# Performance work log

Hardware: AMD Instinct MI355X
Metric: run time of the kernel (lower is better)

The kernel has to match this reference:

```python
import jax, jax.numpy as jnp
import numpy as np

N = 50000
E = 800000
IN_DIM = 128
HID = 128
OUT_DIM = 128
H = 16
D = OUT_DIM // H  # head_dim = 8
EF = 4
RF = 20
KV_IN = 2 * IN_DIM + EF + RF  # 280
EPS = 1e-5


def _layernorm(x, w, b):
    mu = jnp.mean(x, axis=-1, keepdims=True)
    var = jnp.var(x, axis=-1, keepdims=True)
    return (x - mu) * jax.lax.rsqrt(var + EPS) * w + b


def _mlp(x, W1, b1, ln_w, ln_b, W2, b2):
    # Linear -> LayerNorm -> ReLU -> Linear (num_layer=2, norm=True)
    hdn = x @ W1 + b1
    hdn = jax.nn.relu(_layernorm(hdn, ln_w, ln_b))
    return hdn @ W2 + b2


def _lin_init(key, fan_in, fan_out):
    k1, k2 = jax.random.split(key)
    s = 1.0 / np.sqrt(fan_in)
    W = jax.random.uniform(k1, (fan_in, fan_out), jnp.float32, -s, s)
    b = jax.random.uniform(k2, (fan_out,), jnp.float32, -s, s)
    return W, b


def _mlp_params(key, in_dim, hid, out_dim):
    k1, k2 = jax.random.split(key)
    W1, b1 = _lin_init(k1, in_dim, hid)
    W2, b2 = _lin_init(k2, hid, out_dim)
    return W1, b1, jnp.ones((hid,), jnp.float32), jnp.zeros((hid,), jnp.float32), W2, b2


def setup_inputs() -> dict:
    key = jax.random.key(0)
    ks = jax.random.split(key, 10)
    h = jax.random.normal(ks[0], (N, IN_DIM), jnp.float32)
    rel_x = jax.random.normal(ks[1], (E, 3), jnp.float32)
    r_feat = jax.random.normal(ks[2], (E, RF), jnp.float32)
    edge_feat = jax.random.normal(ks[3], (E, EF), jnp.float32)
    edge_index = jax.random.randint(ks[4], (2, E), 0, N, jnp.int64)

    xk = _mlp_params(ks[5], KV_IN, HID, OUT_DIM)
    xv = _mlp_params(ks[6], KV_IN, HID, H)
    xq = _mlp_params(ks[7], IN_DIM, HID, OUT_DIM)
    ew_W, ew_b = _lin_init(ks[8], RF, 1)

    d = {"h": h, "rel_x": rel_x, "r_feat": r_feat, "edge_feat": edge_feat,
         "edge_index": edge_index, "ew_W": ew_W, "ew_b": ew_b}
    for name, p in (("xk", xk), ("xv", xv), ("xq", xq)):
        d[name + "_W1"], d[name + "_b1"], d[name + "_ln_w"], d[name + "_ln_b"], d[name + "_W2"], d[name + "_b2"] = p
    return d


def reference(h, rel_x, r_feat, edge_feat, edge_index,
              ew_W, ew_b,
              xk_W1, xk_b1, xk_ln_w, xk_ln_b, xk_W2, xk_b2,
              xv_W1, xv_b1, xv_ln_w, xv_ln_b, xv_W2, xv_b2,
              xq_W1, xq_b1, xq_ln_w, xq_ln_b, xq_W2, xq_b2):
    src, dst = edge_index[0], edge_index[1]
    hi = h[dst]  # [E, IN_DIM]
    hj = h[src]  # [E, IN_DIM]
    kv_input = jnp.concatenate([edge_feat, r_feat, hi, hj], axis=-1)  # [E, KV_IN]

    k = _mlp(kv_input, xk_W1, xk_b1, xk_ln_w, xk_ln_b, xk_W2, xk_b2).reshape(E, H, D)
    v = _mlp(kv_input, xv_W1, xv_b1, xv_ln_w, xv_ln_b, xv_W2, xv_b2)  # [E, H]
    e_w = jax.nn.sigmoid(r_feat @ ew_W + ew_b)  # [E, 1]
    v = (v * e_w)[:, :, None] * rel_x[:, None, :]  # [E, H, 3]

    q = _mlp(h, xq_W1, xq_b1, xq_ln_w, xq_ln_b, xq_W2, xq_b2).reshape(N, H, D)
    scores = jnp.sum(q[dst] * k, axis=-1) / np.sqrt(D)  # [E, H]

    # scatter_softmax over destination groups
    seg_max = jax.ops.segment_max(scores, dst, num_segments=N)  # [N, H]
    ex = jnp.exp(scores - seg_max[dst])
    denom = jax.ops.segment_sum(ex, dst, num_segments=N)  # [N, H]
    alpha = ex / denom[dst]  # [E, H]

    m = alpha[:, :, None] * v  # [E, H, 3]
    output = jax.ops.segment_sum(m, dst, num_segments=N)  # [N, H, 3]
    return output.mean(axis=1)  # [N, 3]
```

## Files before the change

kernel.cpp:

```cpp
#include <hip/hip_runtime.h>
#include <hip/hip_bf16.h>

#define NN 50000
#define EE 800000
#define ET 32
#define SCB 49

typedef unsigned int u32;
typedef __attribute__((ext_vector_type(8))) short short8;
typedef __attribute__((ext_vector_type(4))) float floatx4;

template<bool BF>
__device__ __forceinline__ float ldf(const void* p, int i){
  if constexpr (BF) return __bfloat162float(((const __hip_bfloat16*)p)[i]);
  else              return ((const float*)p)[i];
}
__device__ __forceinline__ int gidx(const int* ei, int pos, bool i64){
  return i64 ? ei[2*pos] : ei[pos];
}
__device__ __forceinline__ bool det_bf(const void* lnw){
  return ((const u32*)lnw)[0] == 0x3F803F80u;
}
__device__ __forceinline__ bool det_i64(const int* ei){
  return ((ei[1] | ei[3] | ei[5] | ei[7]) == 0);
}

__device__ __forceinline__ unsigned short f2bf(float f){
  u32 u = __float_as_uint(f);
  u32 r = u + 0x7FFFu + ((u>>16)&1u);
  return (unsigned short)(r>>16);
}
__device__ __forceinline__ float bf2f(unsigned short s){
  return __uint_as_float(((u32)s)<<16);
}
__device__ __forceinline__ u32 cvtpk(float lo, float hi){
  u32 r;
  asm("v_cvt_pk_bf16_f32 %0, %1, %2" : "=v"(r) : "v"(lo), "v"(hi));
  return r;
}

__global__ void __launch_bounds__(256)
k_hist(const int* ei, int* cnt){
  int t = blockIdx.x*256 + threadIdx.x;
  if (t >= EE) return;
  bool i64 = det_i64(ei);
  atomicAdd(&cnt[gidx(ei, EE + t, i64)], 1);
}

__global__ void __launch_bounds__(256)
k_scan1(const int* cnt, int* bsum){
  __shared__ int wsum[4];
  int t=threadIdx.x, lane=t&63, wv=t>>6;
  int i0 = blockIdx.x*1024 + t*4;
  int s=0;
  #pragma unroll
  for(int j=0;j<4;j++){ int i=i0+j; s += (i<NN)?cnt[i]:0; }
  #pragma unroll
  for(int d=1;d<64;d<<=1) s += __shfl_xor(s,d);
  if(lane==0) wsum[wv]=s;
  __syncthreads();
  if(t==0) bsum[blockIdx.x]=wsum[0]+wsum[1]+wsum[2]+wsum[3];
}

__global__ void __launch_bounds__(256)
k_scan3(const int* cnt, const int* bsum, int* off){
  __shared__ int wsum[4];
  int t=threadIdx.x, lane=t&63, wv=t>>6;
  int base=0;
  for(int k=0;k<blockIdx.x;k++) base += bsum[k];
  int i0=blockIdx.x*1024 + t*4;
  int v0=(i0+0<NN)?cnt[i0+0]:0;
  int v1=(i0+1<NN)?cnt[i0+1]:0;
  int v2=(i0+2<NN)?cnt[i0+2]:0;
  int v3=(i0+3<NN)?cnt[i0+3]:0;
  int s=v0+v1+v2+v3;
  int sc=s;
  #pragma unroll
  for(int d=1;d<64;d<<=1){ int u=__shfl_up(sc,d); if(lane>=d) sc+=u; }
  if(lane==63) wsum[wv]=sc;
  __syncthreads();
  int wb=base;
  for(int k=0;k<wv;k++) wb+=wsum[k];
  int excl=wb+sc-s;
  if(i0+0<NN) off[i0+0]=excl;
  if(i0+1<NN) off[i0+1]=excl+v0;
  if(i0+2<NN) off[i0+2]=excl+v0+v1;
  if(i0+3<NN) off[i0+3]=excl+v0+v1+v2;
  if (blockIdx.x==SCB-1 && t==0)
    off[NN] = base + wsum[0]+wsum[1]+wsum[2]+wsum[3];
}

template<bool BF>
__device__ void scat_body(const int* ei, bool i64, const int* off, int* cur,
                          const void* rfeat, const void* relx,
                          const void* ewW, const void* ewb, float* blob){
  int t = blockIdx.x*256 + threadIdx.x;
  if (t >= EE) return;
  int d = gidx(ei, EE + t, i64);
  int pos = off[d] + atomicAdd(&cur[d], 1);
  float rf[20];
  if constexpr (!BF){
    const float* rp = (const float*)rfeat + (size_t)t*20;
    #pragma unroll
    for (int q=0;q<5;q++){
      float4 v4 = *(const float4*)(rp + q*4);
      rf[q*4+0]=v4.x; rf[q*4+1]=v4.y; rf[q*4+2]=v4.z; rf[q*4+3]=v4.w;
    }
  } else {
    #pragma unroll
    for (int j=0;j<20;j++) rf[j] = ldf<BF>(rfeat, t*20+j);
  }
  float aw = ldf<BF>(ewb, 0);
  #pragma unroll
  for (int j=0;j<20;j++) aw = fmaf(rf[j], ldf<BF>(ewW,j), aw);
  int4 a; a.x=d; a.y=gidx(ei, t, i64); a.z=t; a.w=0;
  float4 b;
  b.x = (1.f/(1.f + expf(-aw))) * (1.f/16.f);
  b.y = ldf<BF>(relx, t*3+0);
  b.z = ldf<BF>(relx, t*3+1);
  b.w = ldf<BF>(relx, t*3+2);
  ((int4*)blob)[2*(size_t)pos]   = a;
  ((float4*)blob)[2*(size_t)pos+1] = b;
}
__global__ void __launch_bounds__(256)
k_scat(const int* ei, const int* off, int* cur,
       const void* rfeat, const void* relx, const void* ewW, const void* ewb,
       float* blob, const void* lnw){
  bool i64 = det_i64(ei);
  if (det_bf(lnw)) scat_body<true >(ei,i64,off,cur,rfeat,relx,ewW,ewb,blob);
  else             scat_body<false>(ei,i64,off,cur,rfeat,relx,ewW,ewb,blob);
}

__global__ void __launch_bounds__(256)
k_wprep(const void* kW1, const void* vW1, const void* kW2, const void* vW2,
        const void* qW1, const void* qW2,
        unsigned short* w1sh, unsigned short* w1sl,
        unsigned short* w1nh, unsigned short* w1nl,
        unsigned short* w2kh, unsigned short* w2kl,
        unsigned short* w2vh, unsigned short* w2vl,
        unsigned short* w1qh, unsigned short* w1ql,
        unsigned short* w2qh, unsigned short* w2ql, const void* lnw){
  int idx = blockIdx.x*256 + threadIdx.x;
  bool bf = det_bf(lnw);
  {
    int c = idx>>7, k = idx&127;
    int row = (c<256) ? (24+k) : (152+k);
    int cc  = c & 127;
    const void* W = ((c&255)<128) ? kW1 : vW1;
    float f = bf ? __bfloat162float(((const __hip_bfloat16*)W)[row*128+cc]) : ((const float*)W)[row*128+cc];
    unsigned short h = f2bf(f); w1nh[idx]=h; w1nl[idx]=f2bf(f - bf2f(h));
  }
  if (idx < 16384){ int c = idx>>7, k = idx&127;
    { float f = bf ? __bfloat162float(((const __hip_bfloat16*)kW2)[k*128+c]) : ((const float*)kW2)[k*128+c];
      unsigned short h = f2bf(f); w2kh[idx]=h; w2kl[idx]=f2bf(f - bf2f(h)); }
    { float f = bf ? __bfloat162float(((const __hip_bfloat16*)qW1)[k*128+c]) : ((const float*)qW1)[k*128+c];
      unsigned short h = f2bf(f); w1qh[idx]=h; w1ql[idx]=f2bf(f - bf2f(h)); }
    { float f = bf ? __bfloat162float(((const __hip_bfloat16*)qW2)[k*128+c]) : ((const float*)qW2)[k*128+c];
      unsigned short h = f2bf(f); w2qh[idx]=h; w2ql[idx]=f2bf(f - bf2f(h)); }
  }
  if (idx < 2048){ int c = idx>>7, k = idx&127;
    float f = bf ? __bfloat162float(((const __hip_bfloat16*)vW2)[k*16+c]) : ((const float*)vW2)[k*16+c];
    unsigned short h = f2bf(f); w2vh[idx]=h; w2vl[idx]=f2bf(f - bf2f(h)); }
  if (idx < 8192){ int c = idx>>5, k = idx&31;
    float f = 0.f;
    if (k < 24){
      if (c < 128) f = bf ? __bfloat162float(((const __hip_bfloat16*)kW1)[k*128+c]) : ((const float*)kW1)[k*128+c];
      else         f = bf ? __bfloat162float(((const __hip_bfloat16*)vW1)[k*128+(c-128)]) : ((const float*)vW1)[k*128+(c-128)];
    }
    unsigned short h = f2bf(f); w1sh[idx]=h; w1sl[idx]=f2bf(f - bf2f(h)); }
}

template<bool BF>
__device__ void nodeq_body(const void* h,
                           const unsigned short* w1nh, const unsigned short* w1nl,
                           const unsigned short* w1qh, const unsigned short* w1ql,
                           const unsigned short* w2qh, const unsigned short* w2ql,
                           const void* kb1, const void* vb1,
                           const void* qb1, const void* qlnw, const void* qlnb, const void* qb2,
                           float* hkd, float* hks, float* qws,
                           unsigned short* xh, unsigned short* xl,
                           unsigned short* yh, unsigned short* yl,
                           float2 (*lnred)[4]){
  const int t = threadIdx.x;
  const int n0 = blockIdx.x*16;
  const int lane = t&63, w = t>>6;
  const int arow = lane&15, agrp = lane>>4;
  { int nd = t>>4, c8 = (t&15)*8;
    float v[8];
    if constexpr (!BF){
      float4 a = *(const float4*)&((const float*)h)[(n0+nd)*128 + c8];
      float4 b = *(const float4*)&((const float*)h)[(n0+nd)*128 + c8 + 4];
      v[0]=a.x; v[1]=a.y; v[2]=a.z; v[3]=a.w; v[4]=b.x; v[5]=b.y; v[6]=b.z; v[7]=b.w;
    } else {
      short8 raw = *(const short8*)&((const __hip_bfloat16*)h)[(n0+nd)*128 + c8];
      #pragma unroll
      for (int i=0;i<8;i++) v[i] = bf2f((unsigned short)raw[i]);
    }
    short8 hv, lv;
    #pragma unroll
    for (int i=0;i<8;i++){
      unsigned short hh = f2bf(v[i]);
      hv[i] = (short)hh; lv[i] = (short)f2bf(v[i]-bf2f(hh));
    }
    int sidx = (nd*128 + c8) ^ ((nd&7)<<3);
    *(short8*)&xh[sidx] = hv;
    *(short8*)&xl[sidx] = lv;
  }
  __syncthreads();
  { floatx4 acc[8];
    #pragma unroll
    for (int ct=0; ct<8; ct++)
      #pragma unroll
      for (int r=0;r<4;r++) acc[ct][r]=0.f;
    #pragma unroll
    for (int ks=0; ks<4; ks++){
      int aidx = (arow*128 + ks*32 + agrp*8) ^ ((arow&7)<<3);
      short8 Ah = *(const short8*)&xh[aidx];
      short8 Al = *(const short8*)&xl[aidx];
      #pragma unroll
      for (int ct=0; ct<8; ct++){
        int gc = w*128 + ct*16 + arow;
        short8 Bh = *(const short8*)&w1nh[gc*128 + ks*32 + agrp*8];
        short8 Bl = *(const short8*)&w1nl[gc*128 + ks*32 + agrp*8];
        acc[ct] = __builtin_amdgcn_mfma_f32_16x16x32_bf16(Ah, Bh, acc[ct], 0,0,0);
        acc[ct] = __builtin_amdgcn_mfma_f32_16x16x32_bf16(Al, Bh, acc[ct], 0,0,0);
        acc[ct] = __builtin_amdgcn_mfma_f32_16x16x32_bf16(Ah, Bl, acc[ct], 0,0,0);
      }
    }
    if (w < 2){
      #pragma unroll
      for (int ct=0; ct<8; ct++){
        int gc = w*128 + ct*16 + arow;
        float bb = (gc<128) ? ldf<BF>(kb1,gc) : ldf<BF>(vb1,gc-128);
        #pragma unroll
        for (int r=0;r<4;r++) acc[ct][r] += bb;
      }
    }
    float* base = (w<2) ? hkd : hks;
    const int ob = (w&1)*128;
    #pragma unroll
    for (int r=0;r<4;r++){
      int n = n0 + agrp*4 + r;
      float4 lo4 = make_float4(acc[0][r],acc[1][r],acc[2][r],acc[3][r]);
      float4 hi4 = make_float4(acc[4][r],acc[5][r],acc[6][r],acc[7][r]);
      *(float4*)&base[(size_t)n*256 + ob + arow*4]      = lo4;
      *(float4*)&base[(size_t)n*256 + ob + 64 + arow*4] = hi4;
    }
  }
  floatx4 Cq[2];
  #pragma unroll
  for (int nt=0; nt<2; nt++){
    int col = w*32 + nt*16 + arow;
    float bb = ldf<BF>(qb1, col);
    #pragma unroll
    for (int r=0;r<4;r++) Cq[nt][r] = bb;
  }
  #pragma unroll
  for (int ks=0; ks<4; ks++){
    int aidx = (arow*128 + ks*32 + agrp*8) ^ ((arow&7)<<3);
    short8 Ah = *(const short8*)&xh[aidx];
    short8 Al = *(const short8*)&xl[aidx];
    #pragma unroll
    for (int nt=0; nt<2; nt++){
      int col = w*32 + nt*16 + arow;
      short8 Bh = *(const short8*)&w1qh[col*128 + ks*32 + agrp*8];
      short8 Bl = *(const short8*)&w1ql[col*128 + ks*32 + agrp*8];
      Cq[nt] = __builtin_amdgcn_mfma_f32_16x16x32_bf16(Ah, Bh, Cq[nt], 0,0,0);
      Cq[nt] = __builtin_amdgcn_mfma_f32_16x16x32_bf16(Al, Bh, Cq[nt], 0,0,0);
      Cq[nt] = __builtin_amdgcn_mfma_f32_16x16x32_bf16(Ah, Bl, Cq[nt], 0,0,0);
    }
  }
  { float s1[4], s2[4];
    #pragma unroll
    for (int r=0;r<4;r++){ s1[r]=0.f; s2[r]=0.f; }
    #pragma unroll
    for (int nt=0; nt<2; nt++)
      #pragma unroll
      for (int r=0;r<4;r++){ float v=Cq[nt][r]; s1[r]+=v; s2[r]=fmaf(v,v,s2[r]); }
    #pragma unroll
    for (int d=1; d<16; d<<=1){
      #pragma unroll
      for (int r=0;r<4;r++){ s1[r]+=__shfl_xor(s1[r],d); s2[r]+=__shfl_xor(s2[r],d); }
    }
    if (arow==0){
      #pragma unroll
      for (int r=0;r<4;r++) lnred[agrp*4+r][w] = make_float2(s1[r], s2[r]);
    }
  }
  __syncthreads();
  float mu[4], rs[4];
  #pragma unroll
  for (int r=0;r<4;r++){
    int row = agrp*4+r;
    float s=0.f, q=0.f;
    #pragma unroll
    for (int k=0;k<4;k++){ float2 p=lnred[row][k]; s+=p.x; q+=p.y; }
    float m = s*(1.f/128.f);
    mu[r]=m; rs[r]=rsqrtf(q*(1.f/128.f) - m*m + 1e-5f);
  }
  #pragma unroll
  for (int nt=0; nt<2; nt++){
    int col = w*32 + nt*16 + arow;
    float lw = ldf<BF>(qlnw, col), lb = ldf<BF>(qlnb, col);
    #pragma unroll
    for (int r=0;r<4;r++){
      int row = agrp*4+r;
      float v = fmaxf((Cq[nt][r]-mu[r])*rs[r]*lw + lb, 0.f);
      unsigned short hh = f2bf(v);
      int idx = (row*128 + col) ^ ((row&7)<<3);
      yh[idx] = hh;
      yl[idx] = f2bf(v - bf2f(hh));
    }
  }
  __syncthreads();
  floatx4 Co[2];
  #pragma unroll
  for (int nt=0; nt<2; nt++){
    int col = w*32 + nt*16 + arow;
    float bb = ldf<BF>(qb2, col);
    #pragma unroll
    for (int r=0;r<4;r++) Co[nt][r] = bb;
  }
  #pragma unroll
  for (int ks=0; ks<4; ks++){
    int aidx = (arow*128 + ks*32 + agrp*8) ^ ((arow&7)<<3);
    short8 Ah = *(const short8*)&yh[aidx];
    short8 Al = *(const short8*)&yl[aidx];
    #pragma unroll
    for (int nt=0; nt<2; nt++){
      int col = w*32 + nt*16 + arow;
      short8 Bh = *(const short8*)&w2qh[col*128 + ks*32 + agrp*8];
      short8 Bl = *(const short8*)&w2ql[col*128 + ks*32 + agrp*8];
      Co[nt] = __builtin_amdgcn_mfma_f32_16x16x32_bf16(Ah, Bh, Co[nt], 0,0,0);
      Co[nt] = __builtin_amdgcn_mfma_f32_16x16x32_bf16(Al, Bh, Co[nt], 0,0,0);
      Co[nt] = __builtin_amdgcn_mfma_f32_16x16x32_bf16(Ah, Bl, Co[nt], 0,0,0);
    }
  }
  #pragma unroll
  for (int r=0;r<4;r++){
    int n = n0 + agrp*4 + r;
    *(float2*)&qws[(size_t)n*128 + w*32 + arow*2] = make_float2(Co[0][r], Co[1][r]);
  }
}
__global__ void __launch_bounds__(256)
k_nodeq(const void* h,
        const unsigned short* w1nh, const unsigned short* w1nl,
        const unsigned short* w1qh, const unsigned short* w1ql,
        const unsigned short* w2qh, const unsigned short* w2ql,
        const void* kb1, const void* vb1,
        const void* qb1, const void* qlnw, const void* qlnb, const void* qb2,
        float* hkd, float* hks, float* qws){
  __shared__ unsigned short xh[16*128];
  __shared__ unsigned short xl[16*128];
  __shared__ unsigned short yh[16*128];
  __shared__ unsigned short yl[16*128];
  __shared__ float2 lnred[16][4];
  if (det_bf(qlnw)) nodeq_body<true >(h,w1nh,w1nl,w1qh,w1ql,w2qh,w2ql,kb1,vb1,qb1,qlnw,qlnb,qb2,hkd,hks,qws,xh,xl,yh,yl,lnred);
  else              nodeq_body<false>(h,w1nh,w1nl,w1qh,w1ql,w2qh,w2ql,kb1,vb1,qb1,qlnw,qlnb,qb2,hkd,hks,qws,xh,xl,yh,yl,lnred);
}

template<bool BF>
__device__ void edge_body(const void* rfeat, const void* efeat, const float* blob,
                          const void* klnw, const void* klnb,
                          const void* vlnw, const void* vlnb,
                          const void* kb2, const void* vb2,
                          const unsigned short* w1sh, const unsigned short* w1sl,
                          const unsigned short* w2kh, const unsigned short* w2kl,
                          const unsigned short* w2vh, const unsigned short* w2vl,
                          const float* hkd, const float* hks, const float* qws,
                          float* scw, float* vsw,
                          unsigned short* ahi, unsigned short* sfh,
                          int* dste, int* srce, float* ewv,
                          float2 (*lnred)[4], float* sc_lds){
  const int t  = threadIdx.x;
  const int e0 = blockIdx.x*ET;
  const int lane = t&63, w = t>>6;
  const int arow = lane&15, agrp = lane>>4;
  const int* bi = (const int*)blob;

  if (t < ET)             dste[t]     = bi[(size_t)(e0+t)*8 + 0];
  else if (t < 2*ET)      srce[t-ET]  = bi[(size_t)(e0+t-ET)*8 + 1];
  else if (t < 3*ET)      ewv[t-2*ET] = blob[(size_t)(e0+t-2*ET)*8 + 4];
  #pragma unroll
  for (int it=0; it<4; it++){
    int id = it*256+t; int e = id>>5, j = id&31;
    int ge = bi[(size_t)(e0+e)*8 + 2];
    float f = (j<4) ? ldf<BF>(efeat, ge*4+j)
            : (j<24 ? ldf<BF>(rfeat, ge*20+(j-4)) : 0.f);
    sfh[e*40+j] = f2bf(f);
  }
  __syncthreads();

  const int wcol = w*64 + arow;
  const int pbase = w*64 + arow*4;
  floatx4 C[2][4];
  #pragma unroll
  for (int g=0; g<2; g++){
    #pragma unroll
    for (int r=0;r<4;r++){
      int e = g*16 + agrp*4 + r;
      float4 gd = *(const float4*)&hkd[(size_t)(u32)dste[e]*256u + pbase];
      float4 gs = *(const float4*)&hks[(size_t)(u32)srce[e]*256u + pbase];
      C[g][0][r] = gd.x+gs.x; C[g][1][r] = gd.y+gs.y;
      C[g][2][r] = gd.z+gs.z; C[g][3][r] = gd.w+gs.w;
    }
  }
  #pragma unroll
  for (int g=0; g<2; g++){
    short8 Ah = *(const short8*)&sfh[(g*16+arow)*40 + agrp*8];
    #pragma unroll
    for (int nt=0; nt<4; nt++){
      const int col = wcol + nt*16;
      short8 Bh = *(const short8*)&w1sh[col*32 + agrp*8];
      short8 Bl = *(const short8*)&w1sl[col*32 + agrp*8];
      C[g][nt] = __builtin_amdgcn_mfma_f32_16x16x32_bf16(Ah, Bh, C[g][nt], 0,0,0);
      C[g][nt] = __builtin_amdgcn_mfma_f32_16x16x32_bf16(Ah, Bl, C[g][nt], 0,0,0);
    }
  }
  #pragma unroll
  for (int g=0; g<2; g++){
    float s1[4], s2[4];
    #pragma unroll
    for (int r=0;r<4;r++){ s1[r]=0.f; s2[r]=0.f; }
    #pragma unroll
    for (int nt=0; nt<4; nt++)
      #pragma unroll
      for (int r=0;r<4;r++){ float v=C[g][nt][r]; s1[r]+=v; s2[r]=fmaf(v,v,s2[r]); }
    #pragma unroll
    for (int d=1; d<16; d<<=1){
      #pragma unroll
      for (int r=0;r<4;r++){ s1[r]+=__shfl_xor(s1[r],d); s2[r]+=__shfl_xor(s2[r],d); }
    }
    if (arow==0){
      #pragma unroll
      for (int r=0;r<4;r++) lnred[g*16+agrp*4+r][w] = make_float2(s1[r], s2[r]);
    }
  }
  __syncthreads();
  float mu[2][4], rs[2][4];
  { int b = w>>1;
    #pragma unroll
    for (int g=0; g<2; g++)
      #pragma unroll
      for (int r=0;r<4;r++){
        int row = g*16+agrp*4+r;
        float2 p0 = lnred[row][2*b], p1 = lnred[row][2*b+1];
        float s = p0.x+p1.x, q = p0.y+p1.y;
        float m = s*(1.f/128.f);
        mu[g][r]=m; rs[g][r]=rsqrtf(q*(1.f/128.f) - m*m + 1e-5f);
      }
  }
  #pragma unroll
  for (int nt=0; nt<4; nt++){
    const int col = wcol + nt*16;
    const bool kb = (col<128); const int cc = kb?col:col-128;
    float lw = kb?ldf<BF>(klnw,cc):ldf<BF>(vlnw,cc);
    float lb = kb?ldf<BF>(klnb,cc):ldf<BF>(vlnb,cc);
    #pragma unroll
    for (int g=0; g<2; g++){
      float v[4];
      #pragma unroll
      for (int r=0;r<4;r++)
        v[r] = fmaxf((C[g][nt][r]-mu[g][r])*rs[g][r]*lw + lb, 0.f);
      u32 p01 = cvtpk(v[0], v[1]);
      u32 p23 = cvtpk(v[2], v[3]);
      int row0 = g*16 + agrp*4;
      ahi[((row0+0)*256 + col) ^ (((row0+0)&7)<<3)] = (unsigned short)p01;
      ahi[((row0+1)*256 + col) ^ (((row0+1)&7)<<3)] = (unsigned short)(p01>>16);
      ahi[((row0+2)*256 + col) ^ (((row0+2)&7)<<3)] = (unsigned short)p23;
      ahi[((row0+3)*256 + col) ^ (((row0+3)&7)<<3)] = (unsigned short)(p23>>16);
    }
  }
  __syncthreads();

  const int c0 = (2*w+0)*16 + arow;
  const int c1 = (2*w+1)*16 + arow;
  floatx4 Ck[2][2], Cv;
  { float b0=ldf<BF>(kb2,c0), b1v=ldf<BF>(kb2,c1);
    #pragma unroll
    for (int g=0;g<2;g++)
      #pragma unroll
      for (int r=0;r<4;r++){ Ck[g][0][r]=b0; Ck[g][1][r]=b1v; } }
  const bool dov = (w&1);
  const int  gv  = w>>1;
  if (dov){ float bv=ldf<BF>(vb2,arow);
    #pragma unroll
    for (int r=0;r<4;r++) Cv[r]=bv; }
  #pragma unroll
  for (int ks=0; ks<4; ks++){
    short8 B0h = *(const short8*)&w2kh[c0*128 + ks*32 + agrp*8];
    short8 B0l = *(const short8*)&w2kl[c0*128 + ks*32 + agrp*8];
    short8 B1h = *(const short8*)&w2kh[c1*128 + ks*32 + agrp*8];
    short8 B1l = *(const short8*)&w2kl[c1*128 + ks*32 + agrp*8];
    #pragma unroll
    for (int g=0; g<2; g++){
      int aidx = ((g*16+arow)*256 + ks*32 + agrp*8) ^ ((arow&7)<<3);
      short8 Ah = *(const short8*)&ahi[aidx];
      Ck[g][0] = __builtin_amdgcn_mfma_f32_16x16x32_bf16(Ah, B0h, Ck[g][0], 0,0,0);
      Ck[g][0] = __builtin_amdgcn_mfma_f32_16x16x32_bf16(Ah, B0l, Ck[g][0], 0,0,0);
      Ck[g][1] = __builtin_amdgcn_mfma_f32_16x16x32_bf16(Ah, B1h, Ck[g][1], 0,0,0);
      Ck[g][1] = __builtin_amdgcn_mfma_f32_16x16x32_bf16(Ah, B1l, Ck[g][1], 0,0,0);
    }
    if (dov){
      int avidx = ((gv*16+arow)*256 + 128 + ks*32 + agrp*8) ^ ((arow&7)<<3);
      short8 Avh = *(const short8*)&ahi[avidx];
      short8 Bvh = *(const short8*)&w2vh[arow*128 + ks*32 + agrp*8];
      short8 Bvl = *(const short8*)&w2vl[arow*128 + ks*32 + agrp*8];
      Cv = __builtin_amdgcn_mfma_f32_16x16x32_bf16(Avh, Bvh, Cv, 0,0,0);
      Cv = __builtin_amdgcn_mfma_f32_16x16x32_bf16(Avh, Bvl, Cv, 0,0,0);
    }
  }
  if (dov){
    #pragma unroll
    for (int r=0;r<4;r++){
      int row = gv*16 + agrp*4 + r;
      vsw[(size_t)(e0+row)*16 + arow] = Cv[r]*ewv[row];
    }
  }
  #pragma unroll
  for (int g=0; g<2; g++){
    float p0[4], p1[4];
    #pragma unroll
    for (int r=0;r<4;r++){
      int e = g*16 + agrp*4 + r;
      float2 q2 = *(const float2*)&qws[(size_t)(u32)dste[e]*128u + w*32 + arow*2];
      p0[r] = q2.x*Ck[g][0][r];
      p1[r] = q2.y*Ck[g][1][r];
    }
    #pragma unroll
    for (int d=1; d<8; d<<=1){
      #pragma unroll
      for (int r=0;r<4;r++){ p0[r]+=__shfl_xor(p0[r],d); p1[r]+=__shfl_xor(p1[r],d); }
    }
    int j = arow&7;
    float val = (j<4) ? ((j&2)?((j&1)?p0[3]:p0[2]):((j&1)?p0[1]:p0[0]))
                      : ((j&2)?((j&1)?p1[3]:p1[2]):((j&1)?p1[1]:p1[0]));
    int e  = g*16 + agrp*4 + (j&3);
    int hh = (j<4) ? (4*w + (arow>>3)) : (4*w + 2 + (arow>>3));
    sc_lds[e*17 + hh] = val*0.35355339059327373f;
  }
  __syncthreads();
  #pragma unroll
  for (int u=0; u<2; u++){
    int idx = u*256 + t;
    scw[(size_t)e0*16 + idx] = sc_lds[(idx>>4)*17 + (idx&15)];
  }
}
__global__ void __launch_bounds__(256)
k_edge(const void* rfeat, const void* efeat, const float* blob,
       const void* klnw, const void* klnb, const void* vlnw, const void* vlnb,
       const void* kb2, const void* vb2,
       const unsigned short* w1sh, const unsigned short* w1sl,
       const unsigned short* w2kh, const unsigned short* w2kl,
       const unsigned short* w2vh, const unsigned short* w2vl,
       const float* hkd, const float* hks, const float* qws,
       float* scw, float* vsw){
  __shared__ unsigned short ahi[ET*256];
  __shared__ unsigned short sfh[ET*40];
  __shared__ int   dste[ET], srce[ET];
  __shared__ float ewv[ET];
  __shared__ float2 lnred[ET][4];
  __shared__ float sc_lds[ET*17];
  if (det_bf(klnw)) edge_body<true >(rfeat,efeat,blob,klnw,klnb,vlnw,vlnb,kb2,vb2,
                                     w1sh,w1sl,w2kh,w2kl,w2vh,w2vl,hkd,hks,qws,scw,vsw,
                                     ahi,sfh,dste,srce,ewv,lnred,sc_lds);
  else              edge_body<false>(rfeat,efeat,blob,klnw,klnb,vlnw,vlnb,kb2,vb2,
                                     w1sh,w1sl,w2kh,w2kl,w2vh,w2vl,hkd,hks,qws,scw,vsw,
                                     ahi,sfh,dste,srce,ewv,lnred,sc_lds);
}

template<bool BF>
__device__ void soft_body(const int* off, const float* blob,
                          const float* scw, const float* vsw, void* dout){
  const int t=threadIdx.x, lane=t&63, wv=t>>6;
  const int n = blockIdx.x*4 + wv;
  const int lo=off[n], hi=off[n+1];
  if (lo>=hi){
    if (lane<3){
      if constexpr (BF) ((__hip_bfloat16*)dout)[n*3+lane]=__float2bfloat16(0.f);
      else              ((float*)dout)[n*3+lane]=0.f;
    }
    return;
  }
  const int h=lane&15, es=lane>>4;
  float m=-3.4e38f;
  for (int p=lo+es; p<hi; p+=4) m = fmaxf(m, scw[(size_t)p*16+h]);
  m = fmaxf(m, __shfl_xor(m,16));
  m = fmaxf(m, __shfl_xor(m,32));
  float den=0.f, t0=0.f, t1=0.f, t2=0.f;
  for (int p=lo+es; p<hi; p+=4){
    float ex = expf(scw[(size_t)p*16+h]-m);
    den += ex;
    float a = ex * vsw[(size_t)p*16+h];
    float4 rx = ((const float4*)blob)[2*(size_t)p+1];
    t0 = fmaf(a,rx.y,t0); t1 = fmaf(a,rx.z,t1); t2 = fmaf(a,rx.w,t2);
  }
  den += __shfl_xor(den,16);
  den += __shfl_xor(den,32);
  float id = 1.f/den;
  t0*=id; t1*=id; t2*=id;
  #pragma unroll
  for (int d=1; d<64; d<<=1){
    t0+=__shfl_xor(t0,d); t1+=__shfl_xor(t1,d); t2+=__shfl_xor(t2,d);
  }
  if (lane==0){
    if constexpr (BF){
      ((__hip_bfloat16*)dout)[n*3+0]=__float2bfloat16(t0);
      ((__hip_bfloat16*)dout)[n*3+1]=__float2bfloat16(t1);
      ((__hip_bfloat16*)dout)[n*3+2]=__float2bfloat16(t2);
    } else {
      ((float*)dout)[n*3+0]=t0;
      ((float*)dout)[n*3+1]=t1;
      ((float*)dout)[n*3+2]=t2;
    }
  }
}
__global__ void __launch_bounds__(256)
k_soft(const int* off, const float* blob,
       const float* scw, const float* vsw, void* dout, const void* lnw){
  if (det_bf(lnw)) soft_body<true >(off,blob,scw,vsw,dout);
  else             soft_body<false>(off,blob,scw,vsw,dout);
}

extern "C" void kernel_launch(void* const* d_in, const int* in_sizes, int n_in,
                              void* d_out, int out_size, void* d_ws, size_t ws_size,
                              hipStream_t stream){
  const void* h     = d_in[0];
  const void* relx  = d_in[1];
  const void* rfeat = d_in[2];
  const void* efeat = d_in[3];
  const int*  ei    = (const int*)d_in[4];
  const void* ewW   = d_in[5];
  const void* ewb   = d_in[6];
  const void* kW1 = d_in[7],  *kb1 = d_in[8],  *klnw = d_in[9],  *klnb = d_in[10], *kW2 = d_in[11], *kb2 = d_in[12];
  const void* vW1 = d_in[13], *vb1 = d_in[14], *vlnw = d_in[15], *vlnb = d_in[16], *vW2 = d_in[17], *vb2 = d_in[18];
  const void* qW1 = d_in[19], *qb1 = d_in[20], *qlnw = d_in[21], *qlnb = d_in[22], *qW2 = d_in[23], *qb2 = d_in[24];

  float* qws = (float*)d_ws;
  float* hkd = qws + (size_t)NN*128;
  float* hks = hkd + (size_t)NN*256;
  float* scw = hks + (size_t)NN*256;
  float* vsw = scw + (size_t)EE*16;
  float* blob = vsw + (size_t)EE*16;
  int*   cnt = (int*)(blob + (size_t)EE*8);
  int*   cur = cnt + NN;
  int*   off = cur + NN;
  unsigned short* w1sh = (unsigned short*)(off + NN + 64);
  unsigned short* w1sl = w1sh + 8192;
  unsigned short* w1nh = w1sl + 8192;
  unsigned short* w1nl = w1nh + 65536;
  unsigned short* w2kh = w1nl + 65536;
  unsigned short* w2kl = w2kh + 16384;
  unsigned short* w2vh = w2kl + 16384;
  unsigned short* w2vl = w2vh + 2048;
  unsigned short* w1qh = w2vl + 2048;
  unsigned short* w1ql = w1qh + 16384;
  unsigned short* w2qh = w1ql + 16384;
  unsigned short* w2ql = w2qh + 16384;
  int* bsum  = (int*)(w2ql + 16384);

  hipMemsetAsync(cnt, 0, (size_t)2*NN*sizeof(int), stream);
  k_hist<<<(EE+255)/256, 256, 0, stream>>>(ei, cnt);
  k_scan1<<<SCB, 256, 0, stream>>>(cnt, bsum);
  k_scan3<<<SCB, 256, 0, stream>>>(cnt, bsum, off);
  k_scat<<<(EE+255)/256, 256, 0, stream>>>(ei, off, cur, rfeat, relx, ewW, ewb,
                                           blob, klnw);
  k_wprep<<<256, 256, 0, stream>>>(kW1, vW1, kW2, vW2, qW1, qW2,
                                   w1sh, w1sl, w1nh, w1nl, w2kh, w2kl, w2vh, w2vl,
                                   w1qh, w1ql, w2qh, w2ql, klnw);
  k_nodeq<<<NN/16, 256, 0, stream>>>(h, w1nh, w1nl, w1qh, w1ql, w2qh, w2ql,
                                     kb1, vb1, qb1, qlnw, qlnb, qb2,
                                     hkd, hks, qws);
  k_edge<<<EE/ET, 256, 0, stream>>>(rfeat, efeat, blob,
                                    klnw, klnb, vlnw, vlnb, kb2, vb2,
                                    w1sh, w1sl, w2kh, w2kl, w2vh, w2vl,
                                    hkd, hks, qws, scw, vsw);
  k_soft<<<(NN+3)/4, 256, 0, stream>>>(off, blob, scw, vsw, d_out, klnw);
}
```

Before: 767.0 us.

## Double edge tile to 64 edges per block to reuse weight fragments

Raises the edge-kernel tile from 32 to 64 edges per 256-thread block, so each loaded W1/W2 B-fragment feeds four 16-row MFMA groups instead of two. All four waves now compute the value head rather than only odd waves, and the score staging buffer is aliased onto the edge-feature LDS buffer to keep shared memory in check. The intent is to amortize weight loads from global memory and per-block overhead across more edges. The cost is more accumulator registers per thread (C[4][4], Ck[4][2]), which may reduce occupancy, and half as many blocks.

After: 816.8 us. 6.5% more time.

```diff
diff --git a/kernel.cpp b/kernel.cpp
--- a/kernel.cpp
+++ b/kernel.cpp
@@ -3,7 +3,7 @@
 
 #define NN 50000
 #define EE 800000
-#define ET 32
+#define ET 64
 #define SCB 49
 
 typedef unsigned int u32;
@@ -371,18 +371,19 @@
                           float* scw, float* vsw,
                           unsigned short* ahi, unsigned short* sfh,
                           int* dste, int* srce, float* ewv,
-                          float2 (*lnred)[4], float* sc_lds){
+                          float2 (*lnred)[4]){
   const int t  = threadIdx.x;
   const int e0 = blockIdx.x*ET;
   const int lane = t&63, w = t>>6;
   const int arow = lane&15, agrp = lane>>4;
   const int* bi = (const int*)blob;
-
-  if (t < ET)             dste[t]     = bi[(size_t)(e0+t)*8 + 0];
-  else if (t < 2*ET)      srce[t-ET]  = bi[(size_t)(e0+t-ET)*8 + 1];
-  else if (t < 3*ET)      ewv[t-2*ET] = blob[(size_t)(e0+t-2*ET)*8 + 4];
-  #pragma unroll
-  for (int it=0; it<4; it++){
+  float* sc_lds = (float*)sfh;
+
+  if (t < 64)        dste[t]      = bi[(size_t)(e0+t)*8 + 0];
+  else if (t < 128)  srce[t-64]   = bi[(size_t)(e0+t-64)*8 + 1];
+  else if (t < 192)  ewv[t-128]   = blob[(size_t)(e0+t-128)*8 + 4];
+  #pragma unroll
+  for (int it=0; it<8; it++){
     int id = it*256+t; int e = id>>5, j = id&31;
     int ge = bi[(size_t)(e0+e)*8 + 2];
     float f = (j<4) ? ldf<BF>(efeat, ge*4+j)
@@ -393,9 +394,9 @@
 
   const int wcol = w*64 + arow;
   const int pbase = w*64 + arow*4;
-  floatx4 C[2][4];
-  #pragma unroll
-  for (int g=0; g<2; g++){
+  floatx4 C[4][4];
+  #pragma unroll
+  for (int g=0; g<4; g++){
     #pragma unroll
     for (int r=0;r<4;r++){
       int e = g*16 + agrp*4 + r;
@@ -405,20 +406,23 @@
       C[g][2][r] = gd.z+gs.z; C[g][3][r] = gd.w+gs.w;
     }
   }
-  #pragma unroll
-  for (int g=0; g<2; g++){
-    short8 Ah = *(const short8*)&sfh[(g*16+arow)*40 + agrp*8];
+  { short8 Asr[4];
+    #pragma unroll
+    for (int g=0; g<4; g++) Asr[g] = *(const short8*)&sfh[(g*16+arow)*40 + agrp*8];
     #pragma unroll
     for (int nt=0; nt<4; nt++){
       const int col = wcol + nt*16;
       short8 Bh = *(const short8*)&w1sh[col*32 + agrp*8];
       short8 Bl = *(const short8*)&w1sl[col*32 + agrp*8];
-      C[g][nt] = __builtin_amdgcn_mfma_f32_16x16x32_bf16(Ah, Bh, C[g][nt], 0,0,0);
-      C[g][nt] = __builtin_amdgcn_mfma_f32_16x16x32_bf16(Ah, Bl, C[g][nt], 0,0,0);
-    }
-  }
-  #pragma unroll
-  for (int g=0; g<2; g++){
+      #pragma unroll
+      for (int g=0; g<4; g++){
+        C[g][nt] = __builtin_amdgcn_mfma_f32_16x16x32_bf16(Asr[g], Bh, C[g][nt], 0,0,0);
+        C[g][nt] = __builtin_amdgcn_mfma_f32_16x16x32_bf16(Asr[g], Bl, C[g][nt], 0,0,0);
+      }
+    }
+  }
+  #pragma unroll
+  for (int g=0; g<4; g++){
     float s1[4], s2[4];
     #pragma unroll
     for (int r=0;r<4;r++){ s1[r]=0.f; s2[r]=0.f; }
@@ -437,53 +441,49 @@
     }
   }
   __syncthreads();
-  float mu[2][4], rs[2][4];
   { int b = w>>1;
     #pragma unroll
-    for (int g=0; g<2; g++)
+    for (int g=0; g<4; g++){
+      float mu[4], rs[4];
       #pragma unroll
       for (int r=0;r<4;r++){
         int row = g*16+agrp*4+r;
         float2 p0 = lnred[row][2*b], p1 = lnred[row][2*b+1];
         float s = p0.x+p1.x, q = p0.y+p1.y;
         float m = s*(1.f/128.f);
-        mu[g][r]=m; rs[g][r]=rsqrtf(q*(1.f/128.f) - m*m + 1e-5f);
+        mu[r]=m; rs[r]=rsqrtf(q*(1.f/128.f) - m*m + 1e-5f);
       }
-  }
-  #pragma unroll
-  for (int nt=0; nt<4; nt++){
-    const int col = wcol + nt*16;
-    const bool kb = (col<128); const int cc = kb?col:col-128;
-    float lw = kb?ldf<BF>(klnw,cc):ldf<BF>(vlnw,cc);
-    float lb = kb?ldf<BF>(klnb,cc):ldf<BF>(vlnb,cc);
-    #pragma unroll
-    for (int g=0; g<2; g++){
-      float v[4];
-      #pragma unroll
-      for (int r=0;r<4;r++)
-        v[r] = fmaxf((C[g][nt][r]-mu[g][r])*rs[g][r]*lw + lb, 0.f);
-      u32 p01 = cvtpk(v[0], v[1]);
-      u32 p23 = cvtpk(v[2], v[3]);
-      int row0 = g*16 + agrp*4;
-      ahi[((row0+0)*256 + col) ^ (((row0+0)&7)<<3)] = (unsigned short)p01;
-      ahi[((row0+1)*256 + col) ^ (((row0+1)&7)<<3)] = (unsigned short)(p01>>16);
-      ahi[((row0+2)*256 + col) ^ (((row0+2)&7)<<3)] = (unsigned short)p23;
-      ahi[((row0+3)*256 + col) ^ (((row0+3)&7)<<3)] = (unsigned short)(p23>>16);
+      #pragma unroll
+      for (int nt=0; nt<4; nt++){
+        const int col = wcol + nt*16;
+        const bool kb = (col<128); const int cc = kb?col:col-128;
+        float lw = kb?ldf<BF>(klnw,cc):ldf<BF>(vlnw,cc);
+        float lb = kb?ldf<BF>(klnb,cc):ldf<BF>(vlnb,cc);
+        float v[4];
+        #pragma unroll
+        for (int r=0;r<4;r++)
+          v[r] = fmaxf((C[g][nt][r]-mu[r])*rs[r]*lw + lb, 0.f);
+        u32 p01 = cvtpk(v[0], v[1]);
+        u32 p23 = cvtpk(v[2], v[3]);
+        int row0 = g*16 + agrp*4;
+        ahi[((row0+0)*256 + col) ^ (((row0+0)&7)<<3)] = (unsigned short)p01;
+        ahi[((row0+1)*256 + col) ^ (((row0+1)&7)<<3)] = (unsigned short)(p01>>16);
+        ahi[((row0+2)*256 + col) ^ (((row0+2)&7)<<3)] = (unsigned short)p23;
+        ahi[((row0+3)*256 + col) ^ (((row0+3)&7)<<3)] = (unsigned short)(p23>>16);
+      }
     }
   }
   __syncthreads();
 
   const int c0 = (2*w+0)*16 + arow;
   const int c1 = (2*w+1)*16 + arow;
-  floatx4 Ck[2][2], Cv;
+  floatx4 Ck[4][2], Cv;
   { float b0=ldf<BF>(kb2,c0), b1v=ldf<BF>(kb2,c1);
     #pragma unroll
-    for (int g=0;g<2;g++)
+    for (int g=0;g<4;g++)
       #pragma unroll
       for (int r=0;r<4;r++){ Ck[g][0][r]=b0; Ck[g][1][r]=b1v; } }
-  const bool dov = (w&1);
-  const int  gv  = w>>1;
-  if (dov){ float bv=ldf<BF>(vb2,arow);
+  { float bv=ldf<BF>(vb2,arow);
     #pragma unroll
     for (int r=0;r<4;r++) Cv[r]=bv; }
   #pragma unroll
@@ -493,7 +493,7 @@
     short8 B1h = *(const short8*)&w2kh[c1*128 + ks*32 + agrp*8];
     short8 B1l = *(const short8*)&w2kl[c1*128 + ks*32 + agrp*8];
     #pragma unroll
-    for (int g=0; g<2; g++){
+    for (int g=0; g<4; g++){
       int aidx = ((g*16+arow)*256 + ks*32 + agrp*8) ^ ((arow&7)<<3);
       short8 Ah = *(const short8*)&ahi[aidx];
       Ck[g][0] = __builtin_amdgcn_mfma_f32_16x16x32_bf16(Ah, B0h, Ck[g][0], 0,0,0);
@@ -501,8 +501,7 @@
       Ck[g][1] = __builtin_amdgcn_mfma_f32_16x16x32_bf16(Ah, B1h, Ck[g][1], 0,0,0);
       Ck[g][1] = __builtin_amdgcn_mfma_f32_16x16x32_bf16(Ah, B1l, Ck[g][1], 0,0,0);
     }
-    if (dov){
-      int avidx = ((gv*16+arow)*256 + 128 + ks*32 + agrp*8) ^ ((arow&7)<<3);
+    { int avidx = ((w*16+arow)*256 + 128 + ks*32 + agrp*8) ^ ((arow&7)<<3);
       short8 Avh = *(const short8*)&ahi[avidx];
       short8 Bvh = *(const short8*)&w2vh[arow*128 + ks*32 + agrp*8];
       short8 Bvl = *(const short8*)&w2vl[arow*128 + ks*32 + agrp*8];
@@ -510,15 +509,15 @@
       Cv = __builtin_amdgcn_mfma_f32_16x16x32_bf16(Avh, Bvl, Cv, 0,0,0);
     }
   }
-  if (dov){
+  {
     #pragma unroll
     for (int r=0;r<4;r++){
-      int row = gv*16 + agrp*4 + r;
+      int row = w*16 + agrp*4 + r;
       vsw[(size_t)(e0+row)*16 + arow] = Cv[r]*ewv[row];
     }
   }
   #pragma unroll
-  for (int g=0; g<2; g++){
+  for (int g=0; g<4; g++){
     float p0[4], p1[4];
     #pragma unroll
     for (int r=0;r<4;r++){
@@ -541,7 +540,7 @@
   }
   __syncthreads();
   #pragma unroll
-  for (int u=0; u<2; u++){
+  for (int u=0; u<4; u++){
     int idx = u*256 + t;
     scw[(size_t)e0*16 + idx] = sc_lds[(idx>>4)*17 + (idx&15)];
   }
@@ -560,13 +559,12 @@
   __shared__ int   dste[ET], srce[ET];
   __shared__ float ewv[ET];
   __shared__ float2 lnred[ET][4];
-  __shared__ float sc_lds[ET*17];
   if (det_bf(klnw)) edge_body<true >(rfeat,efeat,blob,klnw,klnb,vlnw,vlnb,kb2,vb2,
                                      w1sh,w1sl,w2kh,w2kl,w2vh,w2vl,hkd,hks,qws,scw,vsw,
-                                     ahi,sfh,dste,srce,ewv,lnred,sc_lds);
+                                     ahi,sfh,dste,srce,ewv,lnred);
   else              edge_body<false>(rfeat,efeat,blob,klnw,klnb,vlnw,vlnb,kb2,vb2,
                                      w1sh,w1sl,w2kh,w2kl,w2vh,w2vl,hkd,hks,qws,scw,vsw,
-                                     ahi,sfh,dste,srce,ewv,lnred,sc_lds);
+                                     ahi,sfh,dste,srce,ewv,lnred);
 }
 
 template<bool BF>
```
